# Kernel tuning notes

Hardware: AMD Instinct MI355X
Metric: run time of the kernel (lower is better)

## Reference

```python
import jax, jax.numpy as jnp
import numpy as np

N_NODES = 50000
N_EDGES = 800000
N_OBS = 4
HID = 64
K_HOPS = 5


def setup_inputs() -> dict:
    key = jax.random.key(0)
    ks = jax.random.split(key, 8)
    nodes = jax.random.normal(ks[0], (N_NODES, N_OBS), dtype=jnp.float32)
    edge_src = jax.random.randint(ks[1], (N_EDGES,), 0, N_NODES, dtype=jnp.int32)
    edge_dst = jax.random.randint(ks[2], (N_EDGES,), 0, N_NODES, dtype=jnp.int32)
    edge_weight = jax.random.uniform(ks[3], (N_EDGES,), dtype=jnp.float32)
    # Linear weights stored as (in, out); y = x @ W + b
    W_lift = jax.random.normal(ks[4], (1, HID), dtype=jnp.float32) * 0.5
    b_lift = jax.random.normal(ks[5], (HID,), dtype=jnp.float32) * 0.1
    W_hop = jax.random.normal(ks[6], (HID, HID), dtype=jnp.float32) * (1.0 / np.sqrt(HID))
    b_hop = jax.random.normal(ks[7], (HID,), dtype=jnp.float32) * 0.1
    return {"nodes": nodes, "edge_src": edge_src, "edge_dst": edge_dst,
            "edge_weight": edge_weight, "W_lift": W_lift, "b_lift": b_lift,
            "W_hop": W_hop, "b_hop": b_hop}


def reference(nodes, edge_src, edge_dst, edge_weight, W_lift, b_lift, W_hop, b_hop):
    # lift: (N, O, 1) @ (1, H) + b -> (N, O, H)
    X = nodes[:, :, None] @ W_lift + b_lift

    def hop(X, _):
        # sparse adjacency matmul: agg[d] = sum_{e: dst=d} w_e * X[src_e]
        msgs = edge_weight[:, None, None] * X[edge_src]          # (E, O, H)
        agg = jax.ops.segment_sum(msgs, edge_dst, num_segments=N_NODES)
        # shared Linear (torch [Linear]*k aliases one module) + ReLU
        return jax.nn.relu(agg @ W_hop + b_hop), None

    X, _ = jax.lax.scan(hop, X, None, length=K_HOPS)
    return X  # (N_NODES, N_OBS, HID)
```

## Files before the change

### kernel.cpp

```cpp
#include <hip/hip_runtime.h>
#include <hip/hip_fp16.h>

#define N_NODES 50000
#define N_EDGES 800000
#define N_OBS   4
#define HID     64
#define K_HOPS  5
#define ROW     (N_OBS * HID)
#define NSCAN_BLKS ((N_NODES + 1023) / 1024)

typedef _Float16 f16x8 __attribute__((ext_vector_type(8)));
typedef _Float16 f16x4 __attribute__((ext_vector_type(4)));
typedef float    f32x4 __attribute__((ext_vector_type(4)));

__global__ void zero_kernel(int* __restrict__ p, int n) {
    int i = blockIdx.x * blockDim.x + threadIdx.x;
    if (i < n) p[i] = 0;
}

__global__ void hist_kernel(const int* __restrict__ dst, int* __restrict__ cnt,
                            int* __restrict__ erank) {
    int e = blockIdx.x * blockDim.x + threadIdx.x;
    if (e < N_EDGES) erank[e] = atomicAdd(&cnt[dst[e]], 1);
}

__global__ __launch_bounds__(1024) void scan1_kernel(const int* __restrict__ counts,
                                                     int* __restrict__ bsum) {
    __shared__ int wsum[16];
    const int t = threadIdx.x, lane = t & 63, wid = t >> 6;
    int i = blockIdx.x * 1024 + t;
    int x = (i < N_NODES) ? counts[i] : 0;
    #pragma unroll
    for (int off = 32; off > 0; off >>= 1) x += __shfl_xor(x, off);
    if (lane == 0) wsum[wid] = x;
    __syncthreads();
    if (t == 0) {
        int s = 0;
        #pragma unroll
        for (int j = 0; j < 16; ++j) s += wsum[j];
        bsum[blockIdx.x] = s;
    }
}

__global__ void scan2_kernel(int* __restrict__ bsum) {
    const int t = threadIdx.x;
    int v = (t < NSCAN_BLKS) ? bsum[t] : 0;
    int x = v;
    #pragma unroll
    for (int off = 1; off < 64; off <<= 1) {
        int y = __shfl_up(x, off);
        if (t >= off) x += y;
    }
    if (t < NSCAN_BLKS) bsum[t] = x - v;
}

__global__ __launch_bounds__(1024) void scan3_kernel(const int* __restrict__ counts,
                                                     const int* __restrict__ bsum,
                                                     int* __restrict__ offsets) {
    __shared__ int wsum[16];
    __shared__ int wpre[16];
    const int t = threadIdx.x, lane = t & 63, wid = t >> 6;
    int i = blockIdx.x * 1024 + t;
    int v = (i < N_NODES) ? counts[i] : 0;
    int x = v;
    #pragma unroll
    for (int off = 1; off < 64; off <<= 1) {
        int y = __shfl_up(x, off);
        if (lane >= off) x += y;
    }
    if (lane == 63) wsum[wid] = x;
    __syncthreads();
    if (t < 16) {
        int p = 0;
        for (int j = 0; j < t; ++j) p += wsum[j];
        wpre[t] = p;
    }
    __syncthreads();
    int base = bsum[blockIdx.x];
    int incl = base + x + wpre[wid];
    if (i < N_NODES) offsets[i + 1] = incl;
    if (i == 0) offsets[0] = 0;
}

__global__ void scatter_kernel(const int* __restrict__ src, const int* __restrict__ dst,
                               const float* __restrict__ w, const int* __restrict__ offsets,
                               const int* __restrict__ erank,
                               unsigned int* __restrict__ ecmp) {
    int e = blockIdx.x * blockDim.x + threadIdx.x;
    if (e < N_EDGES) {
        int d = dst[e];
        int p = offsets[d] + erank[e];
        __half hw = __float2half(w[e]);
        ecmp[p] = ((unsigned int)__half_as_ushort(hw) << 16) | (unsigned int)src[e];
    }
}

__global__ void packW_kernel(const float* __restrict__ W, _Float16* __restrict__ Bp) {
    int i = blockIdx.x * 256 + threadIdx.x;
    if (i >= 4096) return;
    int j  = i & 7;
    int l  = (i >> 3) & 63;
    int ks = (i >> 9) & 1;
    int w  = i >> 10;
    int k   = ks * 32 + ((j >> 2) * 16) + ((l >> 4) * 4) + (j & 3);
    int col = w * 16 + (l & 15);
    Bp[i] = (_Float16)W[k * 64 + col];
}

__global__ void wlw_kernel(const float* __restrict__ Wl, const float* __restrict__ bl,
                           const float* __restrict__ W, float* __restrict__ WlW,
                           float* __restrict__ blW) {
    int j = threadIdx.x;
    float a = 0.f, b = 0.f;
    #pragma unroll 8
    for (int h = 0; h < 64; ++h) {
        float wv = W[h * 64 + j];
        a += Wl[h] * wv;
        b += bl[h] * wv;
    }
    WlW[j] = a;
    blW[j] = b;
}

__global__ void hop1_gather_kernel(const int* __restrict__ offsets,
                                   const unsigned int* __restrict__ ecmp,
                                   const float* __restrict__ nodes,
                                   float4* __restrict__ T, float* __restrict__ U) {
    int n = blockIdx.x * blockDim.x + threadIdx.x;
    if (n >= N_NODES) return;
    int s = offsets[n], e = offsets[n + 1];
    float4 t = {0.f, 0.f, 0.f, 0.f};
    float u = 0.f;
    for (int i = s; i < e; ++i) {
        unsigned int p = ecmp[i];
        float w = __half2float(__ushort_as_half((unsigned short)(p >> 16)));
        int sn = (int)(p & 0xffffu);
        float4 nv = ((const float4*)nodes)[sn];
        t.x += w * nv.x; t.y += w * nv.y; t.z += w * nv.z; t.w += w * nv.w;
        u += w;
    }
    T[n] = t;
    U[n] = u;
}

__global__ void hop1_finish_kernel(const float4* __restrict__ T, const float* __restrict__ U,
                                   const float* __restrict__ WlW, const float* __restrict__ blW,
                                   const float* __restrict__ bias, _Float16* __restrict__ X) {
    int i = blockIdx.x * blockDim.x + threadIdx.x;
    const int total = N_NODES * ROW / 4;
    if (i >= total) return;
    int n   = i >> 6;
    int rem = i & 63;
    int o   = rem >> 4;
    int h4  = rem & 15;
    float t = ((const float*)&T[n])[o];
    float u = U[n];
    float4 wv = ((const float4*)WlW)[h4];
    float4 bv = ((const float4*)blW)[h4];
    float4 hv = ((const float4*)bias)[h4];
    f16x4 st;
    st[0] = (_Float16)fmaxf(t * wv.x + u * bv.x + hv.x, 0.f);
    st[1] = (_Float16)fmaxf(t * wv.y + u * bv.y + hv.y, 0.f);
    st[2] = (_Float16)fmaxf(t * wv.z + u * bv.z + hv.z, 0.f);
    st[3] = (_Float16)fmaxf(t * wv.w + u * bv.w + hv.w, 0.f);
    *(f16x4*)(X + ((size_t)o * N_NODES + n) * 64 + h4 * 4) = st;
}

template<int LAST>
__global__ __launch_bounds__(256) void hop_kernel(const int* __restrict__ offsets,
                                                  const unsigned int* __restrict__ ecmp,
                                                  const _Float16* __restrict__ Xin,
                                                  const _Float16* __restrict__ Bp,
                                                  const float* __restrict__ bias,
                                                  _Float16* __restrict__ Xout,
                                                  float* __restrict__ Fout) {
    __shared__ __align__(16) char smem[32 * 68 * 4];
    _Float16 (*As)[72]  = (_Float16(*)[72])smem;
    float    (*Asf)[68] = (float(*)[68])smem;

    const int t = threadIdx.x;
    const int wid = t >> 6, lane = t & 63;
    const int b = blockIdx.x;
    const int xcd = b & 7;
    const int o = xcd >> 1;
    const int g = ((b >> 3) << 1) | (xcd & 1);
    const int n0 = g * 32;
    if (n0 >= N_NODES) return;

    const int g8  = lane >> 3;
    const int sub = lane & 7;
    const int local = wid * 8 + g8;
    const int node = n0 + local;
    const int nc = (node < N_NODES) ? node : N_NODES - 1;
    int sN = offsets[nc];
    int eN = offsets[nc + 1];
    if (node >= N_NODES) eN = sN;
    const int deg = eN - sN;

    const _Float16* __restrict__ Xb = Xin + (size_t)o * (N_NODES * 64);

    f16x8 acc0 = (f16x8)(_Float16)0.0f;
    f16x8 acc1 = (f16x8)(_Float16)0.0f;

    for (int base = 0; base < deg; base += 8) {
        f16x8 r[8];
        _Float16 wh[8];
        #pragma unroll
        for (int q = 0; q < 8; ++q) {
            int idx = base + q;
            int e = sN + ((idx < deg) ? idx : 0);
            unsigned int p = ecmp[e];
            unsigned short wu = (idx < deg) ? (unsigned short)(p >> 16) : (unsigned short)0;
            wh[q] = __builtin_bit_cast(_Float16, wu);
            r[q] = *(const f16x8*)(Xb + (int)(p & 0xffffu) * 64 + sub * 8);
        }
        #pragma unroll
        for (int q = 0; q < 8; q += 2) {
            acc0 += r[q]     * wh[q];
            acc1 += r[q + 1] * wh[q + 1];
        }
    }
    acc0 += acc1;
    *(f16x8*)&As[local][sub * 8] = acc0;
    __syncthreads();

    const int r15 = lane & 15, gq = lane >> 4;
    const int nt  = wid >> 1;
    const int ct0 = (wid & 1) * 2;
    const int arow = nt * 16 + r15;
    f16x8 a0, a1;
    ((f16x4*)&a0)[0] = *(const f16x4*)&As[arow][ 0 + 4 * gq];
    ((f16x4*)&a0)[1] = *(const f16x4*)&As[arow][16 + 4 * gq];
    ((f16x4*)&a1)[0] = *(const f16x4*)&As[arow][32 + 4 * gq];
    ((f16x4*)&a1)[1] = *(const f16x4*)&As[arow][48 + 4 * gq];
    float res[2][4];
    #pragma unroll
    for (int c = 0; c < 2; ++c) {
        const int ct = ct0 + c;
        f16x8 b0 = *(const f16x8*)(Bp + ((size_t)(ct * 2 + 0) * 64 + lane) * 8);
        f16x8 b1 = *(const f16x8*)(Bp + ((size_t)(ct * 2 + 1) * 64 + lane) * 8);
        f32x4 cc = {0.f, 0.f, 0.f, 0.f};
        cc = __builtin_amdgcn_mfma_f32_16x16x32_f16(a0, b0, cc, 0, 0, 0);
        cc = __builtin_amdgcn_mfma_f32_16x16x32_f16(a1, b1, cc, 0, 0, 0);
        const float bv = bias[ct * 16 + r15];
        #pragma unroll
        for (int j = 0; j < 4; ++j) res[c][j] = fmaxf(cc[j] + bv, 0.f);
    }
    __syncthreads();

    #pragma unroll
    for (int c = 0; c < 2; ++c) {
        const int h = (ct0 + c) * 16 + r15;
        #pragma unroll
        for (int j = 0; j < 4; ++j) {
            int ln = nt * 16 + gq * 4 + j;
            if (LAST) Asf[ln][h] = res[c][j];
            else      As[ln][h]  = (_Float16)res[c][j];
        }
    }
    __syncthreads();

    const int wl = t >> 3;
    const int ws = t & 7;
    const int wnode = n0 + wl;
    if (wnode < N_NODES) {
        if (LAST) {
            float4 v0 = *(const float4*)&Asf[wl][ws * 8];
            float4 v1 = *(const float4*)&Asf[wl][ws * 8 + 4];
            float* dst = Fout + (size_t)wnode * ROW + o * 64 + ws * 8;
            *(float4*)dst       = v0;
            *(float4*)(dst + 4) = v1;
        } else {
            f16x8 v = *(const f16x8*)&As[wl][ws * 8];
            *(f16x8*)(Xout + ((size_t)o * N_NODES + wnode) * 64 + ws * 8) = v;
        }
    }
}

extern "C" void kernel_launch(void* const* d_in, const int* in_sizes, int n_in,
                              void* d_out, int out_size, void* d_ws, size_t ws_size,
                              hipStream_t stream) {
    const float* nodes   = (const float*)d_in[0];
    const int*   esrc    = (const int*)d_in[1];
    const int*   edst    = (const int*)d_in[2];
    const float* eweight = (const float*)d_in[3];
    const float* W_lift  = (const float*)d_in[4];
    const float* b_lift  = (const float*)d_in[5];
    const float* W_hop   = (const float*)d_in[6];
    const float* b_hop   = (const float*)d_in[7];

    char* ws = (char*)d_ws;
    _Float16*     X0   = (_Float16*)(ws);
    _Float16*     X1   = (_Float16*)(ws + 25600000);
    unsigned int* ECMP = (unsigned int*)(ws + 51200000);
    int*          OFF  = (int*)(ws + 54400000);
    int*          CNT  = (int*)(ws + 54600064);
    int*          BSUM = (int*)(ws + 54800064);
    _Float16*     BP   = (_Float16*)(ws + 54800320);
    float*        WLW  = (float*)(ws + 54808512);
    float*        BLW  = (float*)(ws + 54808768);
    int*          ERANK = (int*)(ws + 54809024);
    float4*       T    = (float4*)(ws + 54809024);
    float*        U    = (float*)(ws + 55609024);

    zero_kernel<<<(N_NODES + 255) / 256, 256, 0, stream>>>(CNT, N_NODES);
    hist_kernel<<<(N_EDGES + 255) / 256, 256, 0, stream>>>(edst, CNT, ERANK);
    scan1_kernel<<<NSCAN_BLKS, 1024, 0, stream>>>(CNT, BSUM);
    scan2_kernel<<<1, 64, 0, stream>>>(BSUM);
    scan3_kernel<<<NSCAN_BLKS, 1024, 0, stream>>>(CNT, BSUM, OFF);
    scatter_kernel<<<(N_EDGES + 255) / 256, 256, 0, stream>>>(esrc, edst, eweight, OFF, ERANK, ECMP);

    packW_kernel<<<16, 256, 0, stream>>>(W_hop, BP);
    wlw_kernel<<<1, 64, 0, stream>>>(W_lift, b_lift, W_hop, WLW, BLW);

    hop1_gather_kernel<<<(N_NODES + 255) / 256, 256, 0, stream>>>(OFF, ECMP, nodes, T, U);
    hop1_finish_kernel<<<(N_NODES * ROW / 4 + 255) / 256, 256, 0, stream>>>(T, U, WLW, BLW, b_hop, X0);

    const int hopGrid = 8 * 782;
    _Float16* Xi = X0;
    _Float16* Xo = X1;
    for (int hop = 1; hop < K_HOPS; ++hop) {
        if (hop == K_HOPS - 1) {
            hop_kernel<1><<<hopGrid, 256, 0, stream>>>(OFF, ECMP, Xi, BP, b_hop,
                                                       nullptr, (float*)d_out);
        } else {
            hop_kernel<0><<<hopGrid, 256, 0, stream>>>(OFF, ECMP, Xi, BP, b_hop,
                                                       Xo, nullptr);
        }
        _Float16* tmp = Xi; Xi = Xo; Xo = tmp;
    }
}
```

Before: 248.6 us.

## Split CSR by source half to improve gather locality

Builds the CSR with two buckets per destination node, one for sources in the lower half of node ids and one for the upper half. Counts, the scan and the scatter are extended to 2*N_NODES, and the hop kernels loop over both buckets. The goal is better cache locality in the X gathers, since edges reading the same half of X are grouped together. In exchange, the preprocessing scans twice as many entries, each node loads two offset pairs, and the per-bucket loop padding to multiples of 8 adds wasted loads for low-degree nodes.

```diff
diff --git a/kernel.cpp b/kernel.cpp
--- a/kernel.cpp
+++ b/kernel.cpp
@@ -7,7 +7,8 @@
 #define HID     64
 #define K_HOPS  5
 #define ROW     (N_OBS * HID)
-#define NSCAN_BLKS ((N_NODES + 1023) / 1024)
+#define NHALF   (N_NODES / 2)
+#define NSCAN2_BLKS ((2 * N_NODES + 1023) / 1024)
 
 typedef _Float16 f16x8 __attribute__((ext_vector_type(8)));
 typedef _Float16 f16x4 __attribute__((ext_vector_type(4)));
@@ -18,10 +19,13 @@
     if (i < n) p[i] = 0;
 }
 
-__global__ void hist_kernel(const int* __restrict__ dst, int* __restrict__ cnt,
-                            int* __restrict__ erank) {
+__global__ void hist_kernel(const int* __restrict__ src, const int* __restrict__ dst,
+                            int* __restrict__ cnt2, unsigned short* __restrict__ erank) {
     int e = blockIdx.x * blockDim.x + threadIdx.x;
-    if (e < N_EDGES) erank[e] = atomicAdd(&cnt[dst[e]], 1);
+    if (e < N_EDGES) {
+        int half = (src[e] >= NHALF) ? 1 : 0;
+        erank[e] = (unsigned short)atomicAdd(&cnt2[half * N_NODES + dst[e]], 1);
+    }
 }
 
 __global__ __launch_bounds__(1024) void scan1_kernel(const int* __restrict__ counts,
@@ -29,7 +33,7 @@
     __shared__ int wsum[16];
     const int t = threadIdx.x, lane = t & 63, wid = t >> 6;
     int i = blockIdx.x * 1024 + t;
-    int x = (i < N_NODES) ? counts[i] : 0;
+    int x = (i < 2 * N_NODES) ? counts[i] : 0;
     #pragma unroll
     for (int off = 32; off > 0; off >>= 1) x += __shfl_xor(x, off);
     if (lane == 0) wsum[wid] = x;
@@ -44,14 +48,19 @@
 
 __global__ void scan2_kernel(int* __restrict__ bsum) {
     const int t = threadIdx.x;
-    int v = (t < NSCAN_BLKS) ? bsum[t] : 0;
+    const int lane = t & 63, w = t >> 6;
+    __shared__ int w0tot;
+    int v = (t < NSCAN2_BLKS) ? bsum[t] : 0;
     int x = v;
     #pragma unroll
     for (int off = 1; off < 64; off <<= 1) {
         int y = __shfl_up(x, off);
-        if (t >= off) x += y;
-    }
-    if (t < NSCAN_BLKS) bsum[t] = x - v;
+        if (lane >= off) x += y;
+    }
+    if (t == 63) w0tot = x;
+    __syncthreads();
+    if (w == 1) x += w0tot;
+    if (t < NSCAN2_BLKS) bsum[t] = x - v;
 }
 
 __global__ __launch_bounds__(1024) void scan3_kernel(const int* __restrict__ counts,
@@ -61,7 +70,7 @@
     __shared__ int wpre[16];
     const int t = threadIdx.x, lane = t & 63, wid = t >> 6;
     int i = blockIdx.x * 1024 + t;
-    int v = (i < N_NODES) ? counts[i] : 0;
+    int v = (i < 2 * N_NODES) ? counts[i] : 0;
     int x = v;
     #pragma unroll
     for (int off = 1; off < 64; off <<= 1) {
@@ -78,20 +87,21 @@
     __syncthreads();
     int base = bsum[blockIdx.x];
     int incl = base + x + wpre[wid];
-    if (i < N_NODES) offsets[i + 1] = incl;
+    if (i < 2 * N_NODES) offsets[i + 1] = incl;
     if (i == 0) offsets[0] = 0;
 }
 
 __global__ void scatter_kernel(const int* __restrict__ src, const int* __restrict__ dst,
                                const float* __restrict__ w, const int* __restrict__ offsets,
-                               const int* __restrict__ erank,
+                               const unsigned short* __restrict__ erank,
                                unsigned int* __restrict__ ecmp) {
     int e = blockIdx.x * blockDim.x + threadIdx.x;
     if (e < N_EDGES) {
-        int d = dst[e];
-        int p = offsets[d] + erank[e];
+        int s = src[e];
+        int half = (s >= NHALF) ? 1 : 0;
+        int p = offsets[half * N_NODES + dst[e]] + (int)erank[e];
         __half hw = __float2half(w[e]);
-        ecmp[p] = ((unsigned int)__half_as_ushort(hw) << 16) | (unsigned int)src[e];
+        ecmp[p] = ((unsigned int)__half_as_ushort(hw) << 16) | (unsigned int)s;
     }
 }
 
@@ -128,16 +138,20 @@
                                    float4* __restrict__ T, float* __restrict__ U) {
     int n = blockIdx.x * blockDim.x + threadIdx.x;
     if (n >= N_NODES) return;
-    int s = offsets[n], e = offsets[n + 1];
     float4 t = {0.f, 0.f, 0.f, 0.f};
     float u = 0.f;
-    for (int i = s; i < e; ++i) {
-        unsigned int p = ecmp[i];
-        float w = __half2float(__ushort_as_half((unsigned short)(p >> 16)));
-        int sn = (int)(p & 0xffffu);
-        float4 nv = ((const float4*)nodes)[sn];
-        t.x += w * nv.x; t.y += w * nv.y; t.z += w * nv.z; t.w += w * nv.w;
-        u += w;
+    #pragma unroll
+    for (int h2 = 0; h2 < 2; ++h2) {
+        int s = offsets[h2 * N_NODES + n];
+        int e = offsets[h2 * N_NODES + n + 1];
+        for (int i = s; i < e; ++i) {
+            unsigned int p = ecmp[i];
+            float w = __half2float(__ushort_as_half((unsigned short)(p >> 16)));
+            int sn = (int)(p & 0xffffu);
+            float4 nv = ((const float4*)nodes)[sn];
+            t.x += w * nv.x; t.y += w * nv.y; t.z += w * nv.z; t.w += w * nv.w;
+            u += w;
+        }
     }
     T[n] = t;
     U[n] = u;
@@ -192,32 +206,39 @@
     const int local = wid * 8 + g8;
     const int node = n0 + local;
     const int nc = (node < N_NODES) ? node : N_NODES - 1;
-    int sN = offsets[nc];
-    int eN = offsets[nc + 1];
-    if (node >= N_NODES) eN = sN;
-    const int deg = eN - sN;
+    const int sA = offsets[nc];
+    const int eA = offsets[nc + 1];
+    const int sB = offsets[N_NODES + nc];
+    const int eB = offsets[N_NODES + nc + 1];
+    const int degA = (node < N_NODES) ? (eA - sA) : 0;
+    const int degB = (node < N_NODES) ? (eB - sB) : 0;
 
     const _Float16* __restrict__ Xb = Xin + (size_t)o * (N_NODES * 64);
 
     f16x8 acc0 = (f16x8)(_Float16)0.0f;
     f16x8 acc1 = (f16x8)(_Float16)0.0f;
 
-    for (int base = 0; base < deg; base += 8) {
-        f16x8 r[8];
-        _Float16 wh[8];
-        #pragma unroll
-        for (int q = 0; q < 8; ++q) {
-            int idx = base + q;
-            int e = sN + ((idx < deg) ? idx : 0);
-            unsigned int p = ecmp[e];
-            unsigned short wu = (idx < deg) ? (unsigned short)(p >> 16) : (unsigned short)0;
-            wh[q] = __builtin_bit_cast(_Float16, wu);
-            r[q] = *(const f16x8*)(Xb + (int)(p & 0xffffu) * 64 + sub * 8);
-        }
-        #pragma unroll
-        for (int q = 0; q < 8; q += 2) {
-            acc0 += r[q]     * wh[q];
-            acc1 += r[q + 1] * wh[q + 1];
+    #pragma unroll
+    for (int h2 = 0; h2 < 2; ++h2) {
+        const int sN  = h2 ? sB : sA;
+        const int deg = h2 ? degB : degA;
+        for (int base = 0; base < deg; base += 8) {
+            f16x8 r[8];
+            _Float16 wh[8];
+            #pragma unroll
+            for (int q = 0; q < 8; ++q) {
+                int idx = base + q;
+                int e = sN + ((idx < deg) ? idx : 0);
+                unsigned int p = ecmp[e];
+                unsigned short wu = (idx < deg) ? (unsigned short)(p >> 16) : (unsigned short)0;
+                wh[q] = __builtin_bit_cast(_Float16, wu);
+                r[q] = *(const f16x8*)(Xb + (int)(p & 0xffffu) * 64 + sub * 8);
+            }
+            #pragma unroll
+            for (int q = 0; q < 8; q += 2) {
+                acc0 += r[q]     * wh[q];
+                acc1 += r[q + 1] * wh[q + 1];
+            }
         }
     }
     acc0 += acc1;
@@ -261,18 +282,18 @@
     __syncthreads();
 
     const int wl = t >> 3;
-    const int ws = t & 7;
+    const int wsc = t & 7;
     const int wnode = n0 + wl;
     if (wnode < N_NODES) {
         if (LAST) {
-            float4 v0 = *(const float4*)&Asf[wl][ws * 8];
-            float4 v1 = *(const float4*)&Asf[wl][ws * 8 + 4];
-            float* dst = Fout + (size_t)wnode * ROW + o * 64 + ws * 8;
+            float4 v0 = *(const float4*)&Asf[wl][wsc * 8];
+            float4 v1 = *(const float4*)&Asf[wl][wsc * 8 + 4];
+            float* dst = Fout + (size_t)wnode * ROW + o * 64 + wsc * 8;
             *(float4*)dst       = v0;
             *(float4*)(dst + 4) = v1;
         } else {
-            f16x8 v = *(const f16x8*)&As[wl][ws * 8];
-            *(f16x8*)(Xout + ((size_t)o * N_NODES + wnode) * 64 + ws * 8) = v;
+            f16x8 v = *(const f16x8*)&As[wl][wsc * 8];
+            *(f16x8*)(Xout + ((size_t)o * N_NODES + wnode) * 64 + wsc * 8) = v;
         }
     }
 }
@@ -290,24 +311,24 @@
     const float* b_hop   = (const float*)d_in[7];
 
     char* ws = (char*)d_ws;
-    _Float16*     X0   = (_Float16*)(ws);
-    _Float16*     X1   = (_Float16*)(ws + 25600000);
-    unsigned int* ECMP = (unsigned int*)(ws + 51200000);
-    int*          OFF  = (int*)(ws + 54400000);
-    int*          CNT  = (int*)(ws + 54600064);
-    int*          BSUM = (int*)(ws + 54800064);
-    _Float16*     BP   = (_Float16*)(ws + 54800320);
-    float*        WLW  = (float*)(ws + 54808512);
-    float*        BLW  = (float*)(ws + 54808768);
-    int*          ERANK = (int*)(ws + 54809024);
-    float4*       T    = (float4*)(ws + 54809024);
-    float*        U    = (float*)(ws + 55609024);
-
-    zero_kernel<<<(N_NODES + 255) / 256, 256, 0, stream>>>(CNT, N_NODES);
-    hist_kernel<<<(N_EDGES + 255) / 256, 256, 0, stream>>>(edst, CNT, ERANK);
-    scan1_kernel<<<NSCAN_BLKS, 1024, 0, stream>>>(CNT, BSUM);
-    scan2_kernel<<<1, 64, 0, stream>>>(BSUM);
-    scan3_kernel<<<NSCAN_BLKS, 1024, 0, stream>>>(CNT, BSUM, OFF);
+    _Float16*       X0    = (_Float16*)(ws);
+    _Float16*       X1    = (_Float16*)(ws + 25600000);
+    unsigned int*   ECMP  = (unsigned int*)(ws + 51200000);
+    int*            OFF   = (int*)(ws + 54400000);
+    int*            CNT   = (int*)(ws + 54800064);
+    int*            BSUM  = (int*)(ws + 55200064);
+    _Float16*       BP    = (_Float16*)(ws + 55200576);
+    float*          WLW   = (float*)(ws + 55208768);
+    float*          BLW   = (float*)(ws + 55209024);
+    unsigned short* ERANK = (unsigned short*)(ws + 55209280);
+    float4*         T     = (float4*)(ws + 55209280);
+    float*          U     = (float*)(ws + 56009280);
+
+    zero_kernel<<<(2 * N_NODES + 255) / 256, 256, 0, stream>>>(CNT, 2 * N_NODES);
+    hist_kernel<<<(N_EDGES + 255) / 256, 256, 0, stream>>>(esrc, edst, CNT, ERANK);
+    scan1_kernel<<<NSCAN2_BLKS, 1024, 0, stream>>>(CNT, BSUM);
+    scan2_kernel<<<1, 128, 0, stream>>>(BSUM);
+    scan3_kernel<<<NSCAN2_BLKS, 1024, 0, stream>>>(CNT, BSUM, OFF);
     scatter_kernel<<<(N_EDGES + 255) / 256, 256, 0, stream>>>(esrc, edst, eweight, OFF, ERANK, ECMP);
 
     packW_kernel<<<16, 256, 0, stream>>>(W_hop, BP);
```

Measured after the change: 259.3 us. 1.04x slower.
